# Kernel optimization log

Hardware: AMD Instinct MI355X
Metric: run time of the kernel (lower is better)

Reference implementation:

```python
import jax, jax.numpy as jnp
import numpy as np

N, E, D, H, O = 50000, 800000, 128, 128, 64


def setup_inputs() -> dict:
    key = jax.random.key(0)
    ks = jax.random.split(key, 16)
    x = jax.random.normal(ks[0], (N, D), jnp.float32)
    edge_index = jax.random.randint(ks[1], (2, E), 0, N, dtype=jnp.int32).astype(jnp.int64)

    def lin_w(k, out_d, in_d):
        return jax.random.normal(k, (out_d, in_d), jnp.float32) * (1.0 / np.sqrt(in_d))

    return {
        "x": x,
        "edge_index": edge_index,
        # SAGEConv layer 0 (D -> H): lin_l acts on aggregated neighbors (with bias), lin_r on root (no bias)
        "Wl0": lin_w(ks[2], H, D), "bl0": jnp.zeros((H,), jnp.float32), "Wr0": lin_w(ks[3], H, D),
        # SAGEConv layers 1,2 (H -> H)
        "Wl1": lin_w(ks[4], H, H), "bl1": jnp.zeros((H,), jnp.float32), "Wr1": lin_w(ks[5], H, H),
        "Wl2": lin_w(ks[6], H, H), "bl2": jnp.zeros((H,), jnp.float32), "Wr2": lin_w(ks[7], H, H),
        # post_mp: Linear(H,H) -> Dropout -> Linear(H,O)
        "Wp1": lin_w(ks[8], H, H), "bp1": jnp.zeros((H,), jnp.float32),
        "Wp2": lin_w(ks[9], O, H), "bp2": jnp.zeros((O,), jnp.float32),
    }


def _sage_conv(x, src, dst, W_l, b_l, W_r, n_nodes):
    # mean-aggregate neighbor features: scatter messages x[src] onto dst
    msgs = x[src]                                              # [E, F] gather
    agg = jax.ops.segment_sum(msgs, dst, num_segments=n_nodes)  # [N, F]
    cnt = jax.ops.segment_sum(jnp.ones((src.shape[0],), x.dtype), dst, num_segments=n_nodes)
    mean = agg / jnp.maximum(cnt, 1.0)[:, None]
    return mean @ W_l.T + b_l + x @ W_r.T


def reference(x, edge_index, Wl0, bl0, Wr0, Wl1, bl1, Wr1, Wl2, bl2, Wr2, Wp1, bp1, Wp2, bp2):
    src, dst = edge_index[0], edge_index[1]
    n_nodes = x.shape[0]
    layers = [(Wl0, bl0, Wr0), (Wl1, bl1, Wr1), (Wl2, bl2, Wr2)]
    h = x
    for (W_l, b_l, W_r) in layers:
        h = _sage_conv(h, src, dst, W_l, b_l, W_r, n_nodes)
        h = jax.nn.relu(h)
        # dropout is identity at inference (training=False)
    h = h @ Wp1.T + bp1
    h = h @ Wp2.T + bp2
    return jax.nn.log_softmax(h, axis=1)
```

## Files before the change

### kernel.cpp

```cpp
#include <hip/hip_runtime.h>

using s16x8 = __attribute__((ext_vector_type(8))) short;
using f32x4 = __attribute__((ext_vector_type(4))) float;

#define NBUKMAX 512
#define BCAP    3072
#define CHUNK   4096

static __device__ __forceinline__ float bf2f(unsigned short u){
  union { unsigned int i; float f; } v; v.i = ((unsigned)u) << 16; return v.f;
}
static __device__ __forceinline__ unsigned short f2bf(float f){
  union { float f; unsigned int i; } v; v.f = f;
  unsigned int x = v.i;
  return (unsigned short)((x + 0x7fffu + ((x >> 16) & 1u)) >> 16);
}

__global__ __launch_bounds__(256) void k_bscatter(const int* __restrict__ ei, int E,
                                                  int* __restrict__ gcur,
                                                  unsigned int* __restrict__ tmp){
  __shared__ unsigned int pk[CHUNK];
  __shared__ unsigned short bk[CHUNK];
  __shared__ int hist[NBUKMAX];
  __shared__ int cur[NBUKMAX];
  __shared__ int sh64;
  int tid = threadIdx.x;
  if (tid == 0) sh64 = 1;
  for (int j = tid; j < NBUKMAX; j += 256) hist[j] = 0;
  __syncthreads();
  {
    int nc = E < 64 ? E : 64;
    if (tid < nc && ei[2*tid + 1] != 0) sh64 = 0;
  }
  __syncthreads();
  int is64 = sh64;
  int base = blockIdx.x * CHUNK;
  int m = E - base; if (m > CHUNK) m = CHUNK;
  for (int j = tid; j < m; j += 256){
    int i = base + j;
    int s = is64 ? ei[2*(size_t)i] : ei[i];
    int d = is64 ? ei[2*((size_t)E + i)] : ei[(size_t)E + i];
    pk[j] = ((unsigned)(d & 127) << 25) | (unsigned)s;
    int b = d >> 7;
    bk[j] = (unsigned short)b;
    atomicAdd(&hist[b], 1);
  }
  __syncthreads();
  for (int b = tid; b < NBUKMAX; b += 256){
    int r = hist[b];
    cur[b] = (r > 0) ? atomicAdd(&gcur[b], r) : 0;
  }
  __syncthreads();
  for (int j = tid; j < m; j += 256){
    int b = bk[j];
    int p = atomicAdd(&cur[b], 1);
    if (p < BCAP) tmp[(size_t)b*BCAP + p] = pk[j];
  }
}

__global__ __launch_bounds__(256) void k_binfill(const unsigned int* __restrict__ tmp,
                                                 const int* __restrict__ gcur,
                                                 int* __restrict__ rowp,
                                                 int* __restrict__ srcs, int N, int nbk){
  __shared__ int hist[128], cur[128];
  __shared__ unsigned int stg[BCAP];
  __shared__ int lout[BCAP];
  __shared__ int sh_obase;
  int b = blockIdx.x;
  int d0 = b << 7;
  int nd = N - d0; if (nd > 128) nd = 128;
  int n = gcur[b]; if (n > BCAP) n = BCAP; if (n < 0) n = 0;
  int tid = threadIdx.x;
  for (int j = tid; j < 128; j += 256) hist[j] = 0;
  if (tid < 64){
    int lane = tid;
    int carry = 0;
    for (int b0 = 0; b0 <= b; b0 += 64){
      int bb = b0 + lane;
      int sz = 0;
      if (bb < nbk){ sz = gcur[bb]; if (sz > BCAP) sz = BCAP; if (sz < 0) sz = 0; }
      int s = sz;
      #pragma unroll
      for (int off = 1; off < 64; off <<= 1){
        int u = __shfl_up(s, off, 64);
        if (lane >= off) s += u;
      }
      if (bb == b) sh_obase = carry + s - sz;
      carry += __shfl(s, 63, 64);
    }
  }
  __syncthreads();
  int obase = sh_obase;
  const unsigned int* reg = tmp + (size_t)b * BCAP;
  for (int i = tid; i < n; i += 256){
    unsigned int w = reg[i];
    stg[i] = w;
    atomicAdd(&hist[w >> 25], 1);
  }
  __syncthreads();
  if (tid < 64){
    int a  = hist[2*tid];
    int b2 = hist[2*tid+1];
    int ps = a + b2;
    int s = ps;
    #pragma unroll
    for (int off = 1; off < 64; off <<= 1){
      int u = __shfl_up(s, off, 64);
      if (tid >= off) s += u;
    }
    int ep = s - ps;
    cur[2*tid]   = ep;
    cur[2*tid+1] = ep + a;
    if (2*tid   < nd) rowp[d0 + 2*tid]   = obase + ep;
    if (2*tid+1 < nd) rowp[d0 + 2*tid+1] = obase + ep + a;
  }
  if (b == nbk - 1 && tid == 0) rowp[N] = obase + n;
  __syncthreads();
  for (int i = tid; i < n; i += 256){
    unsigned int w = stg[i];
    int p = atomicAdd(&cur[w >> 25], 1);
    lout[p] = (int)(w & 0x1FFFFFFu);
  }
  __syncthreads();
  for (int i = tid; i < n; i += 256) srcs[obase + i] = lout[i];
}

__global__ __launch_bounds__(256) void k_prep(const float* __restrict__ x, unsigned short* __restrict__ xb, int n4, int nx,
                                              const float* __restrict__ w0, const float* __restrict__ w1,
                                              const float* __restrict__ w2, const float* __restrict__ w3,
                                              const float* __restrict__ w4, const float* __restrict__ w5,
                                              unsigned short* __restrict__ o0, unsigned short* __restrict__ o1,
                                              unsigned short* __restrict__ o2, unsigned short* __restrict__ o3,
                                              unsigned short* __restrict__ o4, unsigned short* __restrict__ o5,
                                              const float* __restrict__ Wp1, const float* __restrict__ bp1,
                                              const float* __restrict__ Wp2, const float* __restrict__ bp2,
                                              unsigned short* __restrict__ Wc, float* __restrict__ bc){
  int bx = blockIdx.x;
  if (bx < nx){
    int i = bx*256 + threadIdx.x;
    if (i >= n4) return;
    float4 v = ((const float4*)x)[i];
    ushort4 o; o.x = f2bf(v.x); o.y = f2bf(v.y); o.z = f2bf(v.z); o.w = f2bf(v.w);
    ((ushort4*)xb)[i] = o;
  } else if (bx < nx + 96){
    int w = bx - nx;
    int job = w >> 4, blk = w & 15;
    const float* in; unsigned short* out;
    switch (job){
      case 0: in = w0; out = o0; break;
      case 1: in = w1; out = o1; break;
      case 2: in = w2; out = o2; break;
      case 3: in = w3; out = o3; break;
      case 4: in = w4; out = o4; break;
      default: in = w5; out = o5; break;
    }
    int i = blk*256 + threadIdx.x;
    float4 v = ((const float4*)in)[i];
    ushort4 o; o.x = f2bf(v.x); o.y = f2bf(v.y); o.z = f2bf(v.z); o.w = f2bf(v.w);
    ((ushort4*)out)[i] = o;
  } else {
    int idx = (bx - nx - 96)*256 + threadIdx.x;
    if (idx >= 64*128) return;
    int o = idx >> 7, k = idx & 127;
    float s = 0.f;
    for (int j = 0; j < 128; ++j) s += Wp2[o*128 + j] * Wp1[j*128 + k];
    Wc[o*128 + k] = f2bf(s);
    if (k == 0){
      float t = bp2[o];
      for (int j = 0; j < 128; ++j) t += Wp2[o*128 + j] * bp1[j];
      bc[o] = t;
    }
  }
}

__global__ __launch_bounds__(256) void k_agg(const unsigned short* __restrict__ h,
                                             const int* __restrict__ rowp,
                                             const int* __restrict__ srcs,
                                             unsigned short* __restrict__ mean, int N){
  int node = blockIdx.x*4 + (threadIdx.x >> 6);
  if (node >= N) return;
  int lane = threadIdx.x & 63;
  int g  = lane >> 4;
  int fl = lane & 15;
  int beg = rowp[node], end = rowp[node+1];
  int deg = end - beg;
  if (deg <= 0){
    if (g == 0){
      uint4 z = make_uint4(0,0,0,0);
      *(uint4*)(mean + (size_t)node*128 + fl*8) = z;
    }
    return;
  }
  float acc[8];
  #pragma unroll
  for (int f = 0; f < 8; ++f) acc[f] = 0.f;
  int last = end - 1;
  for (int base = beg; base < end; base += 16){
    int si[4]; float w[4]; uint4 v[4];
    #pragma unroll
    for (int s = 0; s < 4; ++s){
      int sl = base + s*4 + g;
      w[s] = (sl < end) ? 1.f : 0.f;
      si[s] = srcs[sl < end ? sl : last];
    }
    #pragma unroll
    for (int s = 0; s < 4; ++s) v[s] = *(const uint4*)(h + (size_t)si[s]*128 + fl*8);
    #pragma unroll
    for (int s = 0; s < 4; ++s){
      #pragma unroll
      for (int q = 0; q < 4; ++q){
        unsigned int wd = ((const unsigned int*)&v[s])[q];
        acc[2*q]   = fmaf(w[s], bf2f((unsigned short)(wd & 0xffffu)), acc[2*q]);
        acc[2*q+1] = fmaf(w[s], bf2f((unsigned short)(wd >> 16)),     acc[2*q+1]);
      }
    }
  }
  #pragma unroll
  for (int f = 0; f < 8; ++f){
    acc[f] += __shfl_xor(acc[f], 16, 64);
    acc[f] += __shfl_xor(acc[f], 32, 64);
  }
  if (g == 0){
    float inv = 1.f / (float)deg;
    unsigned int o[4];
    #pragma unroll
    for (int q = 0; q < 4; ++q)
      o[q] = ((unsigned int)f2bf(acc[2*q+1]*inv) << 16) | f2bf(acc[2*q]*inv);
    *(uint4*)(mean + (size_t)node*128 + fl*8) = *(uint4*)&o[0];
  }
}

__global__ __launch_bounds__(256) void k_gemm(const unsigned short* __restrict__ mean,
                                              const unsigned short* __restrict__ hin,
                                              const unsigned short* __restrict__ Wl,
                                              const unsigned short* __restrict__ Wr,
                                              const float* __restrict__ bias,
                                              unsigned short* __restrict__ hout, int N){
  __shared__ unsigned short wlds[64*512];
  int wave = threadIdx.x >> 6;
  int lane = threadIdx.x & 63;
  int lr = lane & 15;
  int kg = lane >> 4;

  #pragma unroll
  for (int cc = 0; cc < 16; ++cc){
    int c = wave + cc*4;
    const unsigned short* W = (c < 32) ? Wl : Wr;
    int jt = (c >> 2) & 7, t = c & 3;
    s16x8 v = *(const s16x8*)(W + (size_t)(jt*16 + lr)*128 + t*32 + kg*8);
    *(s16x8*)(wlds + (size_t)c*512 + lane*8) = v;
  }
  __syncthreads();

  int row0 = (blockIdx.x*4 + wave) * 16;
  if (row0 >= N) return;
  int row = row0 + lr; if (row >= N) row = N - 1;

  s16x8 a[8];
  const unsigned short* mrow = mean + (size_t)row*128;
  const unsigned short* hrow = hin  + (size_t)row*128;
  #pragma unroll
  for (int t = 0; t < 4; ++t) a[t]   = *(const s16x8*)(mrow + t*32 + kg*8);
  #pragma unroll
  for (int t = 0; t < 4; ++t) a[4+t] = *(const s16x8*)(hrow + t*32 + kg*8);

  #pragma unroll
  for (int jt = 0; jt < 8; ++jt){
    f32x4 acc = {0.f, 0.f, 0.f, 0.f};
    #pragma unroll
    for (int t = 0; t < 4; ++t){
      s16x8 b = *(const s16x8*)(wlds + (size_t)(jt*4 + t)*512 + lane*8);
      acc = __builtin_amdgcn_mfma_f32_16x16x32_bf16(a[t], b, acc, 0, 0, 0);
    }
    #pragma unroll
    for (int t = 0; t < 4; ++t){
      s16x8 b = *(const s16x8*)(wlds + (size_t)(32 + jt*4 + t)*512 + lane*8);
      acc = __builtin_amdgcn_mfma_f32_16x16x32_bf16(a[4+t], b, acc, 0, 0, 0);
    }
    int ocol = jt*16 + lr;
    float bv = bias[ocol];
    #pragma unroll
    for (int i = 0; i < 4; ++i){
      int orow = row0 + kg*4 + i;
      if (orow < N){
        float v = acc[i] + bv;
        v = fmaxf(v, 0.f);
        hout[(size_t)orow*128 + ocol] = f2bf(v);
      }
    }
  }
}

__global__ __launch_bounds__(256) void k_post(const unsigned short* __restrict__ h,
                                              const unsigned short* __restrict__ Wc,
                                              const float* __restrict__ bc,
                                              float* __restrict__ out, int N){
  int wave = threadIdx.x >> 6;
  int lane = threadIdx.x & 63;
  int row0 = (blockIdx.x*4 + wave) * 16;
  if (row0 >= N) return;
  int lr = lane & 15;
  int kg = lane >> 4;
  int row = row0 + lr; if (row >= N) row = N - 1;

  s16x8 a[4];
  const unsigned short* hrow = h + (size_t)row*128;
  #pragma unroll
  for (int t = 0; t < 4; ++t) a[t] = *(const s16x8*)(hrow + t*32 + kg*8);

  float v[4][4];
  #pragma unroll
  for (int jt = 0; jt < 4; ++jt){
    f32x4 acc = {0.f, 0.f, 0.f, 0.f};
    int j = jt*16 + lr;
    const unsigned short* wrow = Wc + (size_t)j*128;
    #pragma unroll
    for (int t = 0; t < 4; ++t){
      s16x8 b = *(const s16x8*)(wrow + t*32 + kg*8);
      acc = __builtin_amdgcn_mfma_f32_16x16x32_bf16(a[t], b, acc, 0, 0, 0);
    }
    float bv = bc[jt*16 + lr];
    #pragma unroll
    for (int i = 0; i < 4; ++i) v[jt][i] = acc[i] + bv;
  }

  #pragma unroll
  for (int i = 0; i < 4; ++i){
    float m = v[0][i];
    #pragma unroll
    for (int jt = 1; jt < 4; ++jt) m = fmaxf(m, v[jt][i]);
    #pragma unroll
    for (int msk = 1; msk < 16; msk <<= 1) m = fmaxf(m, __shfl_xor(m, msk, 64));
    float s = 0.f;
    #pragma unroll
    for (int jt = 0; jt < 4; ++jt) s += expf(v[jt][i] - m);
    #pragma unroll
    for (int msk = 1; msk < 16; msk <<= 1) s += __shfl_xor(s, msk, 64);
    float lse = m + logf(s);
    int orow = row0 + kg*4 + i;
    if (orow < N){
      #pragma unroll
      for (int jt = 0; jt < 4; ++jt)
        out[(size_t)orow*64 + jt*16 + lr] = v[jt][i] - lse;
    }
  }
}

extern "C" void kernel_launch(void* const* d_in, const int* in_sizes, int n_in,
                              void* d_out, int out_size, void* d_ws, size_t ws_size,
                              hipStream_t stream){
  const int N = in_sizes[0] / 128;
  const int E = in_sizes[1] / 2;
  if (N <= 0 || E <= 0) return;

  const float* x   = (const float*)d_in[0];
  const int*   ei  = (const int*)d_in[1];
  const float* Wl[3] = {(const float*)d_in[2], (const float*)d_in[5], (const float*)d_in[8]};
  const float* bl[3] = {(const float*)d_in[3], (const float*)d_in[6], (const float*)d_in[9]};
  const float* Wr[3] = {(const float*)d_in[4], (const float*)d_in[7], (const float*)d_in[10]};
  const float* Wp1 = (const float*)d_in[11];
  const float* bp1 = (const float*)d_in[12];
  const float* Wp2 = (const float*)d_in[13];
  const float* bp2 = (const float*)d_in[14];
  float* out = (float*)d_out;

  char* p = (char*)d_ws;
  auto alloc = [&](size_t bytes){ char* r = p; p += (bytes + 255) & ~(size_t)255; return r; };
  unsigned short* xb   = (unsigned short*)alloc((size_t)N*128*2);
  unsigned short* hA   = (unsigned short*)alloc((size_t)N*128*2);
  unsigned short* hB   = (unsigned short*)alloc((size_t)N*128*2);
  unsigned short* mean = (unsigned short*)alloc((size_t)N*128*2);
  unsigned short* wlb[3], *wrb[3];
  for (int l = 0; l < 3; ++l){
    wlb[l] = (unsigned short*)alloc(128*128*2);
    wrb[l] = (unsigned short*)alloc(128*128*2);
  }
  unsigned short* wc = (unsigned short*)alloc(64*128*2);
  float* bc   = (float*)alloc(64*4);
  int* rowp   = (int*)alloc((size_t)(N+1)*4);
  int* srcs   = (int*)alloc((size_t)E*4);
  int* gcur   = (int*)alloc((size_t)NBUKMAX*4);
  unsigned int* tmp = (unsigned int*)alloc((size_t)NBUKMAX*BCAP*4);

  int nbk = (N + 127) >> 7;

  hipMemsetAsync(gcur, 0, (size_t)NBUKMAX*4, stream);
  k_bscatter<<<(E + CHUNK - 1)/CHUNK, 256, 0, stream>>>(ei, E, gcur, tmp);
  k_binfill<<<nbk, 256, 0, stream>>>(tmp, gcur, rowp, srcs, N, nbk);

  int n4 = N*128/4;
  int nx = (n4 + 255)/256;
  k_prep<<<nx + 96 + 32, 256, 0, stream>>>(x, xb, n4, nx,
                                           Wl[0], Wr[0], Wl[1], Wr[1], Wl[2], Wr[2],
                                           wlb[0], wrb[0], wlb[1], wrb[1], wlb[2], wrb[2],
                                           Wp1, bp1, Wp2, bp2, wc, bc);

  int waves = (N + 15)/16;
  int gblocks = (waves + 3)/4;
  const unsigned short* hin = xb;
  unsigned short* houts[3] = {hA, hB, hA};
  for (int l = 0; l < 3; ++l){
    k_agg<<<(N + 3)/4, 256, 0, stream>>>(hin, rowp, srcs, mean, N);
    k_gemm<<<gblocks, 256, 0, stream>>>(mean, hin, wlb[l], wrb[l], bl[l], houts[l], N);
    hin = houts[l];
  }
  k_post<<<gblocks, 256, 0, stream>>>(hin, wc, bc, out, N);
}
```

Measured before the change: 209.2 us.

## Process two nodes per wave in aggregation and fuse last GEMM with post-MLP

```diff
diff --git a/kernel.cpp b/kernel.cpp
--- a/kernel.cpp
+++ b/kernel.cpp
@@ -177,56 +177,75 @@
                                              const int* __restrict__ rowp,
                                              const int* __restrict__ srcs,
                                              unsigned short* __restrict__ mean, int N){
-  int node = blockIdx.x*4 + (threadIdx.x >> 6);
-  if (node >= N) return;
+  int wv = blockIdx.x*4 + (threadIdx.x >> 6);
+  int n0 = wv*2;
+  if (n0 >= N) return;
+  int n1 = n0 + 1;
   int lane = threadIdx.x & 63;
   int g  = lane >> 4;
   int fl = lane & 15;
-  int beg = rowp[node], end = rowp[node+1];
-  int deg = end - beg;
-  if (deg <= 0){
-    if (g == 0){
-      uint4 z = make_uint4(0,0,0,0);
-      *(uint4*)(mean + (size_t)node*128 + fl*8) = z;
-    }
-    return;
-  }
-  float acc[8];
-  #pragma unroll
-  for (int f = 0; f < 8; ++f) acc[f] = 0.f;
-  int last = end - 1;
-  for (int base = beg; base < end; base += 16){
-    int si[4]; float w[4]; uint4 v[4];
+  int beg0 = rowp[n0], end0 = rowp[n0+1];
+  int beg1 = beg0, end1 = beg0;
+  if (n1 < N){ beg1 = rowp[n1]; end1 = rowp[n1+1]; }
+  int deg0 = end0 - beg0, deg1 = end1 - beg1;
+  int it0 = (deg0 + 15) >> 4, it1 = (deg1 + 15) >> 4;
+  int it = it0 > it1 ? it0 : it1;
+  int c0 = deg0 > 0 ? end0 - 1 : 0;
+  int c1 = deg1 > 0 ? end1 - 1 : 0;
+  float a0[8], a1[8];
+  #pragma unroll
+  for (int f = 0; f < 8; ++f){ a0[f] = 0.f; a1[f] = 0.f; }
+  for (int t = 0; t < it; ++t){
+    int b0 = beg0 + t*16, b1 = beg1 + t*16;
+    int si0[4], si1[4]; float w0[4], w1[4];
     #pragma unroll
     for (int s = 0; s < 4; ++s){
-      int sl = base + s*4 + g;
-      w[s] = (sl < end) ? 1.f : 0.f;
-      si[s] = srcs[sl < end ? sl : last];
-    }
-    #pragma unroll
-    for (int s = 0; s < 4; ++s) v[s] = *(const uint4*)(h + (size_t)si[s]*128 + fl*8);
+      int sl0 = b0 + s*4 + g;
+      w0[s] = (sl0 < end0) ? 1.f : 0.f;
+      si0[s] = srcs[sl0 < end0 ? sl0 : c0];
+      int sl1 = b1 + s*4 + g;
+      w1[s] = (sl1 < end1) ? 1.f : 0.f;
+      si1[s] = srcs[sl1 < end1 ? sl1 : c1];
+    }
+    uint4 v0[4], v1[4];
+    #pragma unroll
+    for (int s = 0; s < 4; ++s) v0[s] = *(const uint4*)(h + (size_t)si0[s]*128 + fl*8);
+    #pragma unroll
+    for (int s = 0; s < 4; ++s) v1[s] = *(const uint4*)(h + (size_t)si1[s]*128 + fl*8);
     #pragma unroll
     for (int s = 0; s < 4; ++s){
       #pragma unroll
       for (int q = 0; q < 4; ++q){
-        unsigned int wd = ((const unsigned int*)&v[s])[q];
-        acc[2*q]   = fmaf(w[s], bf2f((unsigned short)(wd & 0xffffu)), acc[2*q]);
-        acc[2*q+1] = fmaf(w[s], bf2f((unsigned short)(wd >> 16)),     acc[2*q+1]);
+        unsigned int wd = ((const unsigned int*)&v0[s])[q];
+        a0[2*q]   = fmaf(w0[s], bf2f((unsigned short)(wd & 0xffffu)), a0[2*q]);
+        a0[2*q+1] = fmaf(w0[s], bf2f((unsigned short)(wd >> 16)),     a0[2*q+1]);
+        wd = ((const unsigned int*)&v1[s])[q];
+        a1[2*q]   = fmaf(w1[s], bf2f((unsigned short)(wd & 0xffffu)), a1[2*q]);
+        a1[2*q+1] = fmaf(w1[s], bf2f((unsigned short)(wd >> 16)),     a1[2*q+1]);
       }
     }
   }
   #pragma unroll
   for (int f = 0; f < 8; ++f){
-    acc[f] += __shfl_xor(acc[f], 16, 64);
-    acc[f] += __shfl_xor(acc[f], 32, 64);
+    a0[f] += __shfl_xor(a0[f], 16, 64);
+    a0[f] += __shfl_xor(a0[f], 32, 64);
+    a1[f] += __shfl_xor(a1[f], 16, 64);
+    a1[f] += __shfl_xor(a1[f], 32, 64);
   }
   if (g == 0){
-    float inv = 1.f / (float)deg;
+    float inv0 = deg0 > 0 ? 1.f/(float)deg0 : 0.f;
     unsigned int o[4];
     #pragma unroll
     for (int q = 0; q < 4; ++q)
-      o[q] = ((unsigned int)f2bf(acc[2*q+1]*inv) << 16) | f2bf(acc[2*q]*inv);
-    *(uint4*)(mean + (size_t)node*128 + fl*8) = *(uint4*)&o[0];
+      o[q] = ((unsigned int)f2bf(a0[2*q+1]*inv0) << 16) | f2bf(a0[2*q]*inv0);
+    *(uint4*)(mean + (size_t)n0*128 + fl*8) = *(uint4*)&o[0];
+    if (n1 < N){
+      float inv1 = deg1 > 0 ? 1.f/(float)deg1 : 0.f;
+      #pragma unroll
+      for (int q = 0; q < 4; ++q)
+        o[q] = ((unsigned int)f2bf(a1[2*q+1]*inv1) << 16) | f2bf(a1[2*q]*inv1);
+      *(uint4*)(mean + (size_t)n1*128 + fl*8) = *(uint4*)&o[0];
+    }
   }
 }
 
@@ -291,49 +310,99 @@
   }
 }
 
-__global__ __launch_bounds__(256) void k_post(const unsigned short* __restrict__ h,
-                                              const unsigned short* __restrict__ Wc,
-                                              const float* __restrict__ bc,
-                                              float* __restrict__ out, int N){
+__global__ __launch_bounds__(256) void k_gemmpost(const unsigned short* __restrict__ mean,
+                                                  const unsigned short* __restrict__ hin,
+                                                  const unsigned short* __restrict__ Wl,
+                                                  const unsigned short* __restrict__ Wr,
+                                                  const float* __restrict__ bias,
+                                                  const unsigned short* __restrict__ Wc,
+                                                  const float* __restrict__ bc,
+                                                  float* __restrict__ out, int N){
+  __shared__ unsigned short wlds[64*512];
   int wave = threadIdx.x >> 6;
   int lane = threadIdx.x & 63;
-  int row0 = (blockIdx.x*4 + wave) * 16;
-  if (row0 >= N) return;
   int lr = lane & 15;
   int kg = lane >> 4;
+
+  #pragma unroll
+  for (int cc = 0; cc < 16; ++cc){
+    int c = wave + cc*4;
+    const unsigned short* W = (c < 32) ? Wl : Wr;
+    int jt = (c >> 2) & 7, t = c & 3;
+    s16x8 v = *(const s16x8*)(W + (size_t)(jt*16 + lr)*128 + t*32 + kg*8);
+    *(s16x8*)(wlds + (size_t)c*512 + lane*8) = v;
+  }
+  __syncthreads();
+
+  int row0 = (blockIdx.x*4 + wave) * 16;
   int row = row0 + lr; if (row >= N) row = N - 1;
 
-  s16x8 a[4];
-  const unsigned short* hrow = h + (size_t)row*128;
-  #pragma unroll
-  for (int t = 0; t < 4; ++t) a[t] = *(const s16x8*)(hrow + t*32 + kg*8);
-
-  float v[4][4];
+  s16x8 a[8];
+  const unsigned short* mrow = mean + (size_t)row*128;
+  const unsigned short* hrow = hin  + (size_t)row*128;
+  #pragma unroll
+  for (int t = 0; t < 4; ++t) a[t]   = *(const s16x8*)(mrow + t*32 + kg*8);
+  #pragma unroll
+  for (int t = 0; t < 4; ++t) a[4+t] = *(const s16x8*)(hrow + t*32 + kg*8);
+
+  f32x4 acc2[8];
+  #pragma unroll
+  for (int jt = 0; jt < 8; ++jt){
+    f32x4 acc = {0.f, 0.f, 0.f, 0.f};
+    #pragma unroll
+    for (int t = 0; t < 4; ++t){
+      s16x8 b = *(const s16x8*)(wlds + (size_t)(jt*4 + t)*512 + lane*8);
+      acc = __builtin_amdgcn_mfma_f32_16x16x32_bf16(a[t], b, acc, 0, 0, 0);
+    }
+    #pragma unroll
+    for (int t = 0; t < 4; ++t){
+      s16x8 b = *(const s16x8*)(wlds + (size_t)(32 + jt*4 + t)*512 + lane*8);
+      acc = __builtin_amdgcn_mfma_f32_16x16x32_bf16(a[4+t], b, acc, 0, 0, 0);
+    }
+    acc2[jt] = acc;
+  }
+  __syncthreads();
+
+  unsigned short* tl = wlds + (size_t)wave * (16*136);
+  #pragma unroll
+  for (int jt = 0; jt < 8; ++jt){
+    float bv = bias[jt*16 + lr];
+    #pragma unroll
+    for (int i = 0; i < 4; ++i){
+      float v = fmaxf(acc2[jt][i] + bv, 0.f);
+      tl[(kg*4 + i)*136 + jt*16 + lr] = f2bf(v);
+    }
+  }
+  s16x8 am[4];
+  #pragma unroll
+  for (int t = 0; t < 4; ++t)
+    am[t] = *(const s16x8*)(tl + lr*136 + t*32 + kg*8);
+
+  float vv[4][4];
   #pragma unroll
   for (int jt = 0; jt < 4; ++jt){
     f32x4 acc = {0.f, 0.f, 0.f, 0.f};
-    int j = jt*16 + lr;
-    const unsigned short* wrow = Wc + (size_t)j*128;
+    const unsigned short* wrow = Wc + (size_t)(jt*16 + lr)*128;
     #pragma unroll
     for (int t = 0; t < 4; ++t){
       s16x8 b = *(const s16x8*)(wrow + t*32 + kg*8);
-      acc = __builtin_amdgcn_mfma_f32_16x16x32_bf16(a[t], b, acc, 0, 0, 0);
+      acc = __builtin_amdgcn_mfma_f32_16x16x32_bf16(am[t], b, acc, 0, 0, 0);
     }
     float bv = bc[jt*16 + lr];
     #pragma unroll
-    for (int i = 0; i < 4; ++i) v[jt][i] = acc[i] + bv;
+    for (int i = 0; i < 4; ++i) vv[jt][i] = acc[i] + bv;
   }
 
   #pragma unroll
   for (int i = 0; i < 4; ++i){
-    float m = v[0][i];
-    #pragma unroll
-    for (int jt = 1; jt < 4; ++jt) m = fmaxf(m, v[jt][i]);
+    float m = vv[0][i];
+    #pragma unroll
+    for (int jt = 1; jt < 4; ++jt) m = fmaxf(m, vv[jt][i]);
     #pragma unroll
     for (int msk = 1; msk < 16; msk <<= 1) m = fmaxf(m, __shfl_xor(m, msk, 64));
     float s = 0.f;
     #pragma unroll
-    for (int jt = 0; jt < 4; ++jt) s += expf(v[jt][i] - m);
+    for (int jt = 0; jt < 4; ++jt) s += expf(vv[jt][i] - m);
     #pragma unroll
     for (int msk = 1; msk < 16; msk <<= 1) s += __shfl_xor(s, msk, 64);
     float lse = m + logf(s);
@@ -341,7 +410,7 @@
     if (orow < N){
       #pragma unroll
       for (int jt = 0; jt < 4; ++jt)
-        out[(size_t)orow*64 + jt*16 + lr] = v[jt][i] - lse;
+        out[(size_t)orow*64 + jt*16 + lr] = vv[jt][i] - lse;
     }
   }
 }
@@ -397,12 +466,11 @@
 
   int waves = (N + 15)/16;
   int gblocks = (waves + 3)/4;
-  const unsigned short* hin = xb;
-  unsigned short* houts[3] = {hA, hB, hA};
-  for (int l = 0; l < 3; ++l){
-    k_agg<<<(N + 3)/4, 256, 0, stream>>>(hin, rowp, srcs, mean, N);
-    k_gemm<<<gblocks, 256, 0, stream>>>(mean, hin, wlb[l], wrb[l], bl[l], houts[l], N);
-    hin = houts[l];
-  }
-  k_post<<<gblocks, 256, 0, stream>>>(hin, wc, bc, out, N);
-}
+  int ablocks = (N + 7)/8;
+  k_agg<<<ablocks, 256, 0, stream>>>(xb, rowp, srcs, mean, N);
+  k_gemm<<<gblocks, 256, 0, stream>>>(mean, xb, wlb[0], wrb[0], bl[0], hA, N);
+  k_agg<<<ablocks, 256, 0, stream>>>(hA, rowp, srcs, mean, N);
+  k_gemm<<<gblocks, 256, 0, stream>>>(mean, hA, wlb[1], wrb[1], bl[1], hB, N);
+  k_agg<<<ablocks, 256, 0, stream>>>(hB, rowp, srcs, mean, N);
+  k_gemmpost<<<gblocks, 256, 0, stream>>>(mean, hB, wlb[2], wrb[2], bl[2], wc, bc, out, N);
+}
```

Measured after the change: 212.3 us. Within noise of the previous version (+1.5%).
